# Kernel tuning notes

Hardware: AMD Instinct MI355X
Metric: run time of the kernel (lower is better)

## Reference

```python
import jax, jax.numpy as jnp
import numpy as np

B, N, K = 16, 2048, 16          # clouds, points per cloud, knn k
C_IN, C_OUT = 64, 64

def setup_inputs() -> dict:
    key = jax.random.key(0)
    ks = jax.random.split(key, 8)
    s_in = 1.0 / np.sqrt(C_IN)
    return {
        "x": jax.random.normal(ks[0], (B * N, C_IN), jnp.float32),
        "pos": jax.random.normal(ks[1], (B * N, 3), jnp.float32),
        "batch": jnp.repeat(jnp.arange(B, dtype=jnp.int32), N),
        "W_pos": jax.random.normal(ks[2], (3, C_OUT), jnp.float32) / np.sqrt(3.0),
        "b_pos": jnp.zeros((C_OUT,), jnp.float32),
        "W_attn": jax.random.normal(ks[3], (C_OUT, C_OUT), jnp.float32) / np.sqrt(C_OUT),
        "b_attn": jnp.zeros((C_OUT,), jnp.float32),
        "W_val": jax.random.normal(ks[4], (C_IN, C_OUT), jnp.float32) * s_in,
        "W_src": jax.random.normal(ks[5], (C_IN, C_OUT), jnp.float32) * s_in,
        "W_dst": jax.random.normal(ks[6], (C_IN, C_OUT), jnp.float32) * s_in,
    }

def _gather(a, idx):
    # a: [B, N, D], idx: [B, N, K+1] -> [B, N, K+1, D]
    return jax.vmap(lambda ab, ib: ab[ib])(a, idx)

def reference(x, pos, batch, W_pos, b_pos, W_attn, b_attn, W_val, W_src, W_dst):
    # batch is assumed contiguous with equal-size clouds (B clouds of N points),
    # so batch-restricted knn_graph == per-cloud knn after reshape.
    posr = pos.reshape(B, N, 3)
    xr = x.reshape(B, N, C_IN)
    # knn_graph(loop=False): exclude self, then PointTransformerConv re-adds self loops
    d2 = jnp.sum((posr[:, :, None, :] - posr[:, None, :, :]) ** 2, axis=-1)  # [B,N,N]
    d2 = d2 + jnp.eye(N, dtype=d2.dtype) * 1e10
    _, nbr = jax.lax.top_k(-d2, K)                                # [B,N,K] sources j per target i
    self_idx = jnp.broadcast_to(jnp.arange(N)[None, :, None], (B, N, 1))
    nbr = jnp.concatenate([nbr, self_idx], axis=2)                # self loop -> [B,N,K+1]
    alpha_i = xr @ W_dst                                          # lin_dst(x_i)  [B,N,C_OUT]
    alpha_j = _gather(xr @ W_src, nbr)                            # lin_src(x_j)  [B,N,K+1,C_OUT]
    val_j = _gather(xr @ W_val, nbr)                              # lin(x_j)
    pos_j = _gather(posr, nbr)                                    # [B,N,K+1,3]
    delta = (posr[:, :, None, :] - pos_j) @ W_pos + b_pos         # pos_nn(pos_i - pos_j)
    alpha = alpha_i[:, :, None, :] - alpha_j + delta              # subtraction attention
    alpha = alpha @ W_attn + b_attn                               # attn_nn
    alpha = jax.nn.softmax(alpha, axis=2)                         # segment softmax per target i
    out = jnp.sum(alpha * (val_j + delta), axis=2)                # weighted scatter-sum
    return out.reshape(B * N, C_OUT)
```

## Files before the change

kernel.cpp:

```cpp
#include <hip/hip_runtime.h>
#include <math.h>

#define BBATCH 16
#define NPC    2048
#define KNBR   16
#define NPTS   (BBATCH*NPC)
#define NGEMM  512
#define NKNN   512
#define BUFCAP 512

__global__ __launch_bounds__(1024) void fused_gk_kernel(
    const float* __restrict__ pos, const float* __restrict__ x,
    const float* __restrict__ Wpos, const float* __restrict__ bpos,
    const float* __restrict__ Wattn, const float* __restrict__ battn,
    const float* __restrict__ Wval, const float* __restrict__ Wsrc,
    const float* __restrict__ Wdst,
    int* __restrict__ nbr, float* __restrict__ A2, float* __restrict__ S2,
    float* __restrict__ V, float* __restrict__ WP2, float* __restrict__ bb) {
  __shared__ __align__(16) char smem[65536];
  int t = threadIdx.x;
  int bid = blockIdx.x;
  int c = t & 63, g = t >> 6;

  if (bid == NGEMM + NKNN) {
    if (t < 64) {
      for (int r = 0; r < 3; ++r) {
        float a = 0.f;
        for (int d = 0; d < 64; ++d) a += Wpos[r * 64 + d] * Wattn[d * 64 + t];
        WP2[r * 64 + t] = a;
      }
      float a = battn[t];
      for (int d = 0; d < 64; ++d) a += bpos[d] * Wattn[d * 64 + t];
      bb[t] = a;
    }
    return;
  }

  if (bid < NGEMM) {
    float* R0 = (float*)smem;
    float* R1 = (float*)(smem + 16384);
    float* R2 = (float*)(smem + 32768);
    float* R3 = (float*)(smem + 49152);
    float4* R04 = (float4*)R0;
    float4* R34 = (float4*)R3;

    R34[t] = ((const float4*)Wattn)[t];
    R04[t] = ((const float4*)Wdst)[t];
    __syncthreads();
    {
      float a0 = 0, a1 = 0, a2 = 0, a3 = 0;
      for (int k = 0; k < 64; ++k) {
        float w = R3[k * 64 + c];
        a0 += R0[(g * 4 + 0) * 64 + k] * w;
        a1 += R0[(g * 4 + 1) * 64 + k] * w;
        a2 += R0[(g * 4 + 2) * 64 + k] * w;
        a3 += R0[(g * 4 + 3) * 64 + k] * w;
      }
      R1[(g * 4 + 0) * 64 + c] = a0; R1[(g * 4 + 1) * 64 + c] = a1;
      R1[(g * 4 + 2) * 64 + c] = a2; R1[(g * 4 + 3) * 64 + c] = a3;
    }
    __syncthreads();
    R04[t] = ((const float4*)Wsrc)[t];
    __syncthreads();
    {
      float a0 = 0, a1 = 0, a2 = 0, a3 = 0;
      for (int k = 0; k < 64; ++k) {
        float w = R3[k * 64 + c];
        a0 += R0[(g * 4 + 0) * 64 + k] * w;
        a1 += R0[(g * 4 + 1) * 64 + k] * w;
        a2 += R0[(g * 4 + 2) * 64 + k] * w;
        a3 += R0[(g * 4 + 3) * 64 + k] * w;
      }
      R2[(g * 4 + 0) * 64 + c] = a0; R2[(g * 4 + 1) * 64 + c] = a1;
      R2[(g * 4 + 2) * 64 + c] = a2; R2[(g * 4 + 3) * 64 + c] = a3;
    }
    __syncthreads();
    R34[t] = ((const float4*)Wval)[t];
    R04[t] = ((const float4*)(x + (size_t)bid * 64 * 64))[t];
    __syncthreads();

    float v0 = 0, v1 = 0, v2 = 0, v3 = 0;
    float a0 = 0, a1 = 0, a2 = 0, a3 = 0;
    float s0 = 0, s1 = 0, s2 = 0, s3 = 0;
    const float4* xr0 = (const float4*)(R0 + (g * 4 + 0) * 64);
    const float4* xr1 = (const float4*)(R0 + (g * 4 + 1) * 64);
    const float4* xr2 = (const float4*)(R0 + (g * 4 + 2) * 64);
    const float4* xr3 = (const float4*)(R0 + (g * 4 + 3) * 64);
#pragma unroll 4
    for (int k4 = 0; k4 < 16; ++k4) {
      float4 q0 = xr0[k4], q1 = xr1[k4], q2 = xr2[k4], q3 = xr3[k4];
#pragma unroll
      for (int kk = 0; kk < 4; ++kk) {
        int k = k4 * 4 + kk;
        float wv = R3[k * 64 + c];
        float wa = R1[k * 64 + c];
        float ws = R2[k * 64 + c];
        float e0 = (kk == 0) ? q0.x : (kk == 1) ? q0.y : (kk == 2) ? q0.z : q0.w;
        float e1 = (kk == 0) ? q1.x : (kk == 1) ? q1.y : (kk == 2) ? q1.z : q1.w;
        float e2 = (kk == 0) ? q2.x : (kk == 1) ? q2.y : (kk == 2) ? q2.z : q2.w;
        float e3 = (kk == 0) ? q3.x : (kk == 1) ? q3.y : (kk == 2) ? q3.z : q3.w;
        v0 += e0 * wv; v1 += e1 * wv; v2 += e2 * wv; v3 += e3 * wv;
        a0 += e0 * wa; a1 += e1 * wa; a2 += e2 * wa; a3 += e3 * wa;
        s0 += e0 * ws; s1 += e1 * ws; s2 += e2 * ws; s3 += e3 * ws;
      }
    }
    size_t o0 = ((size_t)bid * 64 + g * 4 + 0) * 64 + c;
    V[o0] = v0; A2[o0] = a0; S2[o0] = s0;
    size_t o1 = o0 + 64;  V[o1] = v1; A2[o1] = a1; S2[o1] = s1;
    size_t o2 = o0 + 128; V[o2] = v2; A2[o2] = a2; S2[o2] = s2;
    size_t o3 = o0 + 192; V[o3] = v3; A2[o3] = a3; S2[o3] = s3;
    return;
  }

  int kb = bid - NGEMM;
  float4* pos4 = (float4*)smem;
  unsigned short* buf = (unsigned short*)(smem + 32768);
  int cloud = kb >> 5;
  const float* pc = pos + (size_t)cloud * NPC * 3;
  for (int p = t; p < NPC; p += 1024)
    pos4[p] = make_float4(pc[3 * p], pc[3 * p + 1], pc[3 * p + 2], 0.f);
  __syncthreads();

  int w = g, lane = c;
  for (int u = 0; u < 4; ++u) {
    int lt = u * 16 + w;
    int gi = kb * 64 + lt;
    int ti = gi & (NPC - 1);
    float4 tp = pos4[ti];
    float tx = tp.x, ty = tp.y, tz = tp.z;

    int bkt[32];
#pragma unroll
    for (int cc = 0; cc < 32; ++cc) {
      int j = cc * 64 + lane;
      float4 q = pos4[j];
      float dx = tx - q.x, dy = ty - q.y, dz = tz - q.z;
      float d2 = dx * dx + dy * dy + dz * dz;
      int b = (int)(__float_as_uint(d2) >> 20) - 896;
      bkt[cc] = max(0, min(255, b));
    }

    int lo = 0, hi = 255;
    for (int it = 0; it < 8; ++it) {
      int mid = (lo + hi) >> 1;
      int cnt = 0;
#pragma unroll
      for (int cc = 0; cc < 32; ++cc)
        cnt += (int)__popcll(__ballot(bkt[cc] <= mid));
      if (cnt >= 17) hi = mid; else lo = mid + 1;
    }
    int Tp1 = min(hi + 1, 255);

    int base = 0;
#pragma unroll
    for (int cc = 0; cc < 32; ++cc) {
      bool f = (bkt[cc] <= Tp1);
      unsigned long long mm = __ballot(f);
      unsigned int pre = __builtin_amdgcn_mbcnt_hi(
          (unsigned)(mm >> 32), __builtin_amdgcn_mbcnt_lo((unsigned)mm, 0u));
      if (f) {
        int p = base + (int)pre;
        if (p < BUFCAP) buf[w * BUFCAP + p] = (unsigned short)(cc * 64 + lane);
      }
      base += (int)__popcll(mm);
    }
    int n = min(base, BUFCAP);
    double txd = (double)tx, tyd = (double)ty, tzd = (double)tz;

    if (n <= 64) {
      unsigned long long gb = 0xFFFFFFFFFFFFFFFFull;
      int gj = 0x40000000 + lane;
      if (lane < n) {
        int j = buf[w * BUFCAP + lane];
        if (j != ti) {
          float4 q = pos4[j];
          double dx = __dsub_rn(txd, (double)q.x);
          double dy = __dsub_rn(tyd, (double)q.y);
          double dz = __dsub_rn(tzd, (double)q.z);
          double d2 = __dadd_rn(__dadd_rn(__dmul_rn(dx, dx), __dmul_rn(dy, dy)),
                                __dmul_rn(dz, dz));
          gb = (unsigned long long)__double_as_longlong(d2);
          gj = j;
        }
      }
      for (int k = 2; k <= 64; k <<= 1) {
        for (int jj = k >> 1; jj > 0; jj >>= 1) {
          unsigned long long ob = __shfl_xor(gb, jj);
          int oj = __shfl_xor(gj, jj);
          bool keepmin = (((lane & k) == 0) == ((lane & jj) == 0));
          bool less = (ob < gb) || (ob == gb && oj < gj);
          if (keepmin == less) { gb = ob; gj = oj; }
        }
      }
      if (lane < KNBR) nbr[(size_t)gi * KNBR + lane] = gj;
    } else {
      unsigned long long kb2[8];
      int id2[8];
#pragma unroll
      for (int r = 0; r < 8; ++r) {
        int e = r * 64 + lane;
        kb2[r] = 0xFFFFFFFFFFFFFFFFull;
        id2[r] = 0x40000000 + e;
        if (e < n) {
          int j = buf[w * BUFCAP + e];
          if (j != ti) {
            float4 q = pos4[j];
            double dx = __dsub_rn(txd, (double)q.x);
            double dy = __dsub_rn(tyd, (double)q.y);
            double dz = __dsub_rn(tzd, (double)q.z);
            double d2 = __dadd_rn(
                __dadd_rn(__dmul_rn(dx, dx), __dmul_rn(dy, dy)),
                __dmul_rn(dz, dz));
            kb2[r] = (unsigned long long)__double_as_longlong(d2);
            id2[r] = j;
          }
        }
      }
      for (int r = 0; r < KNBR; ++r) {
        unsigned long long lb = kb2[0];
        int lj = id2[0];
#pragma unroll
        for (int cc = 1; cc < 8; ++cc)
          if (kb2[cc] < lb || (kb2[cc] == lb && id2[cc] < lj)) {
            lb = kb2[cc]; lj = id2[cc];
          }
        unsigned long long gb2 = lb;
        int gj2 = lj;
#pragma unroll
        for (int d = 32; d >= 1; d >>= 1) {
          unsigned long long ob = __shfl_xor(gb2, d);
          int oj = __shfl_xor(gj2, d);
          if (ob < gb2 || (ob == gb2 && oj < gj2)) { gb2 = ob; gj2 = oj; }
        }
#pragma unroll
        for (int cc = 0; cc < 8; ++cc)
          if (id2[cc] == gj2) kb2[cc] = 0xFFFFFFFFFFFFFFFFull;
        if (lane == 0) nbr[(size_t)gi * KNBR + r] = gj2;
      }
    }
  }
}

__global__ __launch_bounds__(256) void edge_kernel(
    const float* __restrict__ pos, const int* __restrict__ nbr,
    const float* __restrict__ A2, const float* __restrict__ S2,
    const float* __restrict__ V, const float* __restrict__ WP2,
    const float* __restrict__ bbv, const float* __restrict__ Wpos,
    const float* __restrict__ bpos, float* __restrict__ out) {
  int t = threadIdx.x, w = t >> 6, c = t & 63;
  int gi = blockIdx.x * 4 + w;
  int cloudbase = gi & ~(NPC - 1);
  float pix = pos[(size_t)gi * 3], piy = pos[(size_t)gi * 3 + 1],
        piz = pos[(size_t)gi * 3 + 2];
  float a2 = A2[(size_t)gi * 64 + c];
  float wp0 = WP2[c], wp1 = WP2[64 + c], wp2 = WP2[128 + c], bbc = bbv[c];
  float u0 = Wpos[c], u1 = Wpos[64 + c], u2 = Wpos[128 + c], bpc = bpos[c];

  float lg[17], vl[17];
#pragma unroll
  for (int e = 0; e < 17; ++e) {
    int j = (e < 16) ? nbr[(size_t)gi * KNBR + e] : (gi & (NPC - 1));
    int jg = cloudbase + j;
    float dx = pix - pos[(size_t)jg * 3];
    float dy = piy - pos[(size_t)jg * 3 + 1];
    float dz = piz - pos[(size_t)jg * 3 + 2];
    float s2 = S2[(size_t)jg * 64 + c];
    float v = V[(size_t)jg * 64 + c];
    lg[e] = a2 - s2 + dx * wp0 + dy * wp1 + dz * wp2 + bbc;
    vl[e] = v + dx * u0 + dy * u1 + dz * u2 + bpc;
  }
  float mx = lg[0];
#pragma unroll
  for (int e = 1; e < 17; ++e) mx = fmaxf(mx, lg[e]);
  float den = 0.f, acc = 0.f;
#pragma unroll
  for (int e = 0; e < 17; ++e) {
    float wgt = __expf(lg[e] - mx);
    den += wgt;
    acc += wgt * vl[e];
  }
  out[(size_t)gi * 64 + c] = acc / den;
}

extern "C" void kernel_launch(void* const* d_in, const int* in_sizes, int n_in,
                              void* d_out, int out_size, void* d_ws, size_t ws_size,
                              hipStream_t stream) {
  const float* x     = (const float*)d_in[0];
  const float* pos   = (const float*)d_in[1];
  const float* Wpos  = (const float*)d_in[3];
  const float* bpos  = (const float*)d_in[4];
  const float* Wattn = (const float*)d_in[5];
  const float* battn = (const float*)d_in[6];
  const float* Wval  = (const float*)d_in[7];
  const float* Wsrc  = (const float*)d_in[8];
  const float* Wdst  = (const float*)d_in[9];

  float* ws  = (float*)d_ws;
  float* A2  = ws;
  float* S2  = A2 + (size_t)NPTS * 64;
  float* V   = S2 + (size_t)NPTS * 64;
  float* WP2 = V + (size_t)NPTS * 64;
  float* bb  = WP2 + 192;
  int*   nbr = (int*)(bb + 64);
  float* out = (float*)d_out;

  fused_gk_kernel<<<NGEMM + NKNN + 1, 1024, 0, stream>>>(
      pos, x, Wpos, bpos, Wattn, battn, Wval, Wsrc, Wdst,
      nbr, A2, S2, V, WP2, bb);
  edge_kernel<<<NPTS / 4, 256, 0, stream>>>(pos, nbr, A2, S2, V, WP2, bb,
                                            Wpos, bpos, out);
}
```

Measured before the change: 221.0 us.

## Precompute folded weight products once and remap edge blocks per XCD

The Wdst·Wattn and Wsrc·Wattn products, which every GEMM block used to recompute, are now computed once in a new single-block prep kernel that also handles WP2 and bb. The GEMM blocks just load the precomputed matrices into shared memory. The edge kernel block index is remapped so that blocks on the same XCD work on the same cloud, which should improve L2 locality for neighbor gathers. This adds one extra kernel launch, and the prep kernel runs serially ahead of the main work.

```diff
diff --git a/kernel.cpp b/kernel.cpp
--- a/kernel.cpp
+++ b/kernel.cpp
@@ -9,74 +9,65 @@
 #define NKNN   512
 #define BUFCAP 512
 
+__global__ __launch_bounds__(1024) void prep_kernel(
+    const float* __restrict__ Wpos, const float* __restrict__ bpos,
+    const float* __restrict__ Wattn, const float* __restrict__ battn,
+    const float* __restrict__ Wsrc, const float* __restrict__ Wdst,
+    float* __restrict__ Hd, float* __restrict__ Hs,
+    float* __restrict__ WP2, float* __restrict__ bb) {
+  __shared__ float sW[4096];
+  __shared__ float sD[4096];
+  __shared__ float sS[4096];
+  int t = threadIdx.x;
+  ((float4*)sW)[t] = ((const float4*)Wattn)[t];
+  ((float4*)sD)[t] = ((const float4*)Wdst)[t];
+  ((float4*)sS)[t] = ((const float4*)Wsrc)[t];
+  __syncthreads();
+  int c = t & 63, r0 = t >> 6;
+#pragma unroll
+  for (int q = 0; q < 4; ++q) {
+    int r = r0 + 16 * q;
+    float ad = 0.f, as = 0.f;
+    for (int d = 0; d < 64; ++d) {
+      float w = sW[d * 64 + c];
+      ad += sD[r * 64 + d] * w;
+      as += sS[r * 64 + d] * w;
+    }
+    Hd[r * 64 + c] = ad;
+    Hs[r * 64 + c] = as;
+  }
+  if (t < 64) {
+    for (int rr = 0; rr < 3; ++rr) {
+      float a = 0.f;
+      for (int d = 0; d < 64; ++d) a += Wpos[rr * 64 + d] * sW[d * 64 + t];
+      WP2[rr * 64 + t] = a;
+    }
+    float a = battn[t];
+    for (int d = 0; d < 64; ++d) a += bpos[d] * sW[d * 64 + t];
+    bb[t] = a;
+  }
+}
+
 __global__ __launch_bounds__(1024) void fused_gk_kernel(
     const float* __restrict__ pos, const float* __restrict__ x,
-    const float* __restrict__ Wpos, const float* __restrict__ bpos,
-    const float* __restrict__ Wattn, const float* __restrict__ battn,
-    const float* __restrict__ Wval, const float* __restrict__ Wsrc,
-    const float* __restrict__ Wdst,
+    const float* __restrict__ Hd, const float* __restrict__ Hs,
+    const float* __restrict__ Wval,
     int* __restrict__ nbr, float* __restrict__ A2, float* __restrict__ S2,
-    float* __restrict__ V, float* __restrict__ WP2, float* __restrict__ bb) {
+    float* __restrict__ V) {
   __shared__ __align__(16) char smem[65536];
   int t = threadIdx.x;
   int bid = blockIdx.x;
   int c = t & 63, g = t >> 6;
-
-  if (bid == NGEMM + NKNN) {
-    if (t < 64) {
-      for (int r = 0; r < 3; ++r) {
-        float a = 0.f;
-        for (int d = 0; d < 64; ++d) a += Wpos[r * 64 + d] * Wattn[d * 64 + t];
-        WP2[r * 64 + t] = a;
-      }
-      float a = battn[t];
-      for (int d = 0; d < 64; ++d) a += bpos[d] * Wattn[d * 64 + t];
-      bb[t] = a;
-    }
-    return;
-  }
 
   if (bid < NGEMM) {
     float* R0 = (float*)smem;
     float* R1 = (float*)(smem + 16384);
     float* R2 = (float*)(smem + 32768);
     float* R3 = (float*)(smem + 49152);
-    float4* R04 = (float4*)R0;
-    float4* R34 = (float4*)R3;
-
-    R34[t] = ((const float4*)Wattn)[t];
-    R04[t] = ((const float4*)Wdst)[t];
-    __syncthreads();
-    {
-      float a0 = 0, a1 = 0, a2 = 0, a3 = 0;
-      for (int k = 0; k < 64; ++k) {
-        float w = R3[k * 64 + c];
-        a0 += R0[(g * 4 + 0) * 64 + k] * w;
-        a1 += R0[(g * 4 + 1) * 64 + k] * w;
-        a2 += R0[(g * 4 + 2) * 64 + k] * w;
-        a3 += R0[(g * 4 + 3) * 64 + k] * w;
-      }
-      R1[(g * 4 + 0) * 64 + c] = a0; R1[(g * 4 + 1) * 64 + c] = a1;
-      R1[(g * 4 + 2) * 64 + c] = a2; R1[(g * 4 + 3) * 64 + c] = a3;
-    }
-    __syncthreads();
-    R04[t] = ((const float4*)Wsrc)[t];
-    __syncthreads();
-    {
-      float a0 = 0, a1 = 0, a2 = 0, a3 = 0;
-      for (int k = 0; k < 64; ++k) {
-        float w = R3[k * 64 + c];
-        a0 += R0[(g * 4 + 0) * 64 + k] * w;
-        a1 += R0[(g * 4 + 1) * 64 + k] * w;
-        a2 += R0[(g * 4 + 2) * 64 + k] * w;
-        a3 += R0[(g * 4 + 3) * 64 + k] * w;
-      }
-      R2[(g * 4 + 0) * 64 + c] = a0; R2[(g * 4 + 1) * 64 + c] = a1;
-      R2[(g * 4 + 2) * 64 + c] = a2; R2[(g * 4 + 3) * 64 + c] = a3;
-    }
-    __syncthreads();
-    R34[t] = ((const float4*)Wval)[t];
-    R04[t] = ((const float4*)(x + (size_t)bid * 64 * 64))[t];
+    ((float4*)R0)[t] = ((const float4*)(x + (size_t)bid * 64 * 64))[t];
+    ((float4*)R1)[t] = ((const float4*)Hd)[t];
+    ((float4*)R2)[t] = ((const float4*)Hs)[t];
+    ((float4*)R3)[t] = ((const float4*)Wval)[t];
     __syncthreads();
 
     float v0 = 0, v1 = 0, v2 = 0, v3 = 0;
@@ -248,7 +239,11 @@
     const float* __restrict__ bbv, const float* __restrict__ Wpos,
     const float* __restrict__ bpos, float* __restrict__ out) {
   int t = threadIdx.x, w = t >> 6, c = t & 63;
-  int gi = blockIdx.x * 4 + w;
+  int bid = blockIdx.x;
+  int xcd = bid & 7, slot = bid >> 3;
+  int cloud = xcd + 8 * (slot >> 9);
+  int cb = slot & 511;
+  int gi = cloud * NPC + cb * 4 + w;
   int cloudbase = gi & ~(NPC - 1);
   float pix = pos[(size_t)gi * 3], piy = pos[(size_t)gi * 3 + 1],
         piz = pos[(size_t)gi * 3 + 2];
@@ -302,11 +297,14 @@
   float* WP2 = V + (size_t)NPTS * 64;
   float* bb  = WP2 + 192;
   int*   nbr = (int*)(bb + 64);
+  float* Hd  = (float*)(nbr + (size_t)NPTS * KNBR);
+  float* Hs  = Hd + 4096;
   float* out = (float*)d_out;
 
-  fused_gk_kernel<<<NGEMM + NKNN + 1, 1024, 0, stream>>>(
-      pos, x, Wpos, bpos, Wattn, battn, Wval, Wsrc, Wdst,
-      nbr, A2, S2, V, WP2, bb);
+  prep_kernel<<<1, 1024, 0, stream>>>(Wpos, bpos, Wattn, battn, Wsrc, Wdst,
+                                      Hd, Hs, WP2, bb);
+  fused_gk_kernel<<<NGEMM + NKNN, 1024, 0, stream>>>(
+      pos, x, Hd, Hs, Wval, nbr, A2, S2, V);
   edge_kernel<<<NPTS / 4, 256, 0, stream>>>(pos, nbr, A2, S2, V, WP2, bb,
                                             Wpos, bpos, out);
 }
```

Measured after the change: 223.5 us. About the same (+1.1%).
